# Optimization experiments

Measured on AMD Instinct MI355X. Metric: run time of the kernel, lower is better.

The kernel has to match this reference:

```python
import jax, jax.numpy as jnp
import numpy as np

B, S, D_IN = 16, 512, 768
HID, OUT = 64, 12
NEG = 1e12


def setup_inputs() -> dict:
    key = jax.random.key(0)
    k1, k2, k3 = jax.random.split(key, 3)
    x = jax.random.normal(k1, (B, S, D_IN), dtype=jnp.float32)
    mask = jnp.ones((B, S), dtype=jnp.float32)
    W = jax.random.normal(k2, (D_IN, HID * OUT * 2), dtype=jnp.float32) * 0.02
    b = jax.random.normal(k3, (HID * OUT * 2,), dtype=jnp.float32) * 0.02
    return {"x": x, "mask": mask, "W": W, "b": b}


def reference(x, mask, W, b):
    Bb, Ss, _ = x.shape
    h, out = HID, OUT
    # QKV-style projection, split into `out` heads of 2h each
    proj = (x @ W + b).reshape(Bb, Ss, out, 2 * h)  # [b, s, out, 2h]
    qw, kw = proj[..., :h], proj[..., h:]           # [b, s, out, h]

    # Sinusoidal position embedding (merge='zero'): interleaved sin/cos
    pos_ids = jnp.arange(Ss, dtype=x.dtype)
    inv_freq = jnp.power(10000.0, -2.0 * jnp.arange(h // 2, dtype=x.dtype) / h)
    ang = pos_ids[:, None] * inv_freq               # [s, h/2]
    sin, cos = jnp.sin(ang), jnp.cos(ang)
    # torch: pos[..., None, 1::2].repeat(1,1,1,2) -> TILED (not interleaved)
    cos_pos = jnp.concatenate([cos, cos], axis=-1)[None, :, None, :]  # [1, s, 1, h]
    sin_pos = jnp.concatenate([sin, sin], axis=-1)[None, :, None, :]

    def rope(w):
        # stack([-w_odd, w_even], -1).reshape -> interleaved rotation partner
        w2 = jnp.stack([-w[..., 1::2], w[..., ::2]], axis=-1).reshape(w.shape)
        return w * cos_pos + w2 * sin_pos

    qw = rope(qw)
    kw = rope(kw)

    logits = jnp.einsum('bmhd,bnhd->bhmn', qw, kw)  # [b, out, s, s]

    pad = mask[:, None, None, :]                    # broadcast over [b, out, s, s]
    logits = logits * pad - (1.0 - pad) * NEG

    tril = jnp.tril(jnp.ones((Ss, Ss), dtype=logits.dtype), -1)
    logits = logits - tril * NEG

    return logits / (h ** 0.5)
```

## Files before the change

### kernel.cpp

```cpp
#include <hip/hip_runtime.h>
#include <stdint.h>

#define DIN   768
#define NPROJ 1536
#define SEQ   512
#define NHEAD 12
#define NBATCH 16
#define NEGV  1000000000000.0f

typedef short bf16x8 __attribute__((ext_vector_type(8)));
typedef float f32x4  __attribute__((ext_vector_type(4)));

__device__ __forceinline__ unsigned short f2bf(float f) {
    union { float f; unsigned int u; } v; v.f = f;
    return (unsigned short)((v.u + 0x7FFFu + ((v.u >> 16) & 1u)) >> 16);
}
__device__ __forceinline__ float bf2f(unsigned short u) {
    union { unsigned int u; float f; } v; v.u = ((unsigned int)u) << 16;
    return v.f;
}

__global__ __launch_bounds__(256) void k_xcast(const float* __restrict__ X,
                                               unsigned short* __restrict__ Xb) {
    int i = (blockIdx.x * 256 + threadIdx.x) * 4;
    float4 v = *(const float4*)&X[i];
    short4 s;
    s.x = (short)f2bf(v.x); s.y = (short)f2bf(v.y);
    s.z = (short)f2bf(v.z); s.w = (short)f2bf(v.w);
    *(short4*)&Xb[i] = s;
}

__global__ __launch_bounds__(256) void k_wt(const float* __restrict__ W,
                                            unsigned short* __restrict__ Wt) {
    __shared__ unsigned short T[64][72];
    const int n0 = blockIdx.x * 64, k0 = blockIdx.y * 64;
    const int tid = threadIdx.x;
#pragma unroll
    for (int it = 0; it < 4; it++) {
        int c = tid + it * 256;
        int kl = c >> 4, nl = (c & 15) * 4;
        float4 v = *(const float4*)&W[(size_t)(k0 + kl) * NPROJ + n0 + nl];
        T[nl + 0][kl] = f2bf(v.x);
        T[nl + 1][kl] = f2bf(v.y);
        T[nl + 2][kl] = f2bf(v.z);
        T[nl + 3][kl] = f2bf(v.w);
    }
    __syncthreads();
#pragma unroll
    for (int it = 0; it < 2; it++) {
        int c = tid + it * 256;
        int nl = c >> 3, kb = (c & 7) * 8;
        *(int4*)&Wt[(size_t)(n0 + nl) * DIN + k0 + kb] = *(int4*)&T[nl][kb];
    }
}

template <bool PRE>
__global__ __launch_bounds__(256) void k_gemm(const float* __restrict__ X,
                                              const unsigned short* __restrict__ Xb,
                                              const unsigned short* __restrict__ Wt,
                                              const float* __restrict__ bias,
                                              unsigned short* __restrict__ P) {
    __shared__ unsigned short smem[2 * 128 * 72];
    unsigned short* sA = smem;
    unsigned short* sB = smem + 128 * 72;
    const int tid = threadIdx.x;
    const int m0 = blockIdx.y * 128, n0 = blockIdx.x * 128;
    const int lane = tid & 63, w = tid >> 6;
    const int q = lane >> 4, r = lane & 15;
    const int wm = w >> 1, wn = w & 1;
    f32x4 acc[4][4];
#pragma unroll
    for (int i = 0; i < 4; i++)
#pragma unroll
        for (int j = 0; j < 4; j++) acc[i][j] = (f32x4){0.f, 0.f, 0.f, 0.f};

    for (int k0 = 0; k0 < DIN; k0 += 64) {
        __syncthreads();
        if (PRE) {
#pragma unroll
            for (int it = 0; it < 4; it++) {
                int c = tid + it * 256;
                int row = c >> 3, col = (c & 7) * 8;
                *(int4*)&sA[row * 72 + col] =
                    *(const int4*)&Xb[(size_t)(m0 + row) * DIN + k0 + col];
            }
        } else {
#pragma unroll
            for (int it = 0; it < 8; it++) {
                int c = tid + it * 256;
                int row = c >> 4, col = (c & 15) * 4;
                float4 v = *(const float4*)&X[(size_t)(m0 + row) * DIN + k0 + col];
                short4 sv;
                sv.x = (short)f2bf(v.x); sv.y = (short)f2bf(v.y);
                sv.z = (short)f2bf(v.z); sv.w = (short)f2bf(v.w);
                *(short4*)&sA[row * 72 + col] = sv;
            }
        }
#pragma unroll
        for (int it = 0; it < 4; it++) {
            int c = tid + it * 256;
            int row = c >> 3, col = (c & 7) * 8;
            *(int4*)&sB[row * 72 + col] =
                *(const int4*)&Wt[(size_t)(n0 + row) * DIN + k0 + col];
        }
        __syncthreads();
#pragma unroll
        for (int kk = 0; kk < 64; kk += 32) {
            bf16x8 af[4], bfr[4];
#pragma unroll
            for (int t = 0; t < 4; t++)
                af[t] = *(const bf16x8*)&sA[(wm * 64 + t * 16 + r) * 72 + kk + q * 8];
#pragma unroll
            for (int t = 0; t < 4; t++)
                bfr[t] = *(const bf16x8*)&sB[(wn * 64 + t * 16 + r) * 72 + kk + q * 8];
#pragma unroll
            for (int tm = 0; tm < 4; tm++)
#pragma unroll
                for (int tn = 0; tn < 4; tn++)
                    acc[tm][tn] = __builtin_amdgcn_mfma_f32_16x16x32_bf16(
                        af[tm], bfr[tn], acc[tm][tn], 0, 0, 0);
        }
    }
    float bb[4];
#pragma unroll
    for (int tn = 0; tn < 4; tn++) bb[tn] = bias[n0 + wn * 64 + tn * 16 + r];
    __syncthreads();
    unsigned short* sT = smem;
#pragma unroll
    for (int tm = 0; tm < 4; tm++) {
        int rowb = wm * 64 + tm * 16 + q * 4;
#pragma unroll
        for (int tn = 0; tn < 4; tn++) {
            int col = wn * 64 + tn * 16 + r;
#pragma unroll
            for (int i = 0; i < 4; i++)
                sT[(rowb + i) * 136 + col] = f2bf(acc[tm][tn][i] + bb[tn]);
        }
    }
    __syncthreads();
#pragma unroll
    for (int it = 0; it < 8; it++) {
        int c = tid + it * 256;
        int row = c >> 4, colb = (c & 15) * 8;
        *(int4*)&P[(size_t)(m0 + row) * NPROJ + n0 + colb] =
            *(int4*)&sT[row * 136 + colb];
    }
}

__global__ __launch_bounds__(256) void k_rope(unsigned short* __restrict__ P) {
    const int s = blockIdx.x;
    const int tid = threadIdx.x;
    __shared__ float cs[32], sn[32];
    if (tid < 32) {
        const float C = 0.41524101186092034f;
        float a = (float)s * exp2f(-(float)tid * C);
        sincosf(a, &sn[tid], &cs[tid]);
    }
    __syncthreads();
#pragma unroll
    for (int it = 0; it < 12; it++) {
        int idx = tid + it * 256;
        int bb = idx / 192, c = idx % 192;
        unsigned short* p = P + (size_t)(bb * SEQ + s) * NPROJ + c * 8;
        union { int4 v; unsigned short u[8]; } pk;
        pk.v = *(const int4*)p;
        int d0 = (c & 7) * 8;
        float wv[8];
#pragma unroll
        for (int j = 0; j < 8; j++) wv[j] = bf2f(pk.u[j]);
#pragma unroll
        for (int pr = 0; pr < 4; pr++) {
            int je = (d0 + 2 * pr) & 31;
            int jo = je + 1;
            float oe = wv[2 * pr] * cs[je] - wv[2 * pr + 1] * sn[je];
            float oo = wv[2 * pr + 1] * cs[jo] + wv[2 * pr] * sn[jo];
            pk.u[2 * pr]     = f2bf(oe);
            pk.u[2 * pr + 1] = f2bf(oo);
        }
        *(int4*)p = pk.v;
    }
}

__global__ __launch_bounds__(256) void k_attn(const unsigned short* __restrict__ P,
                                              const float* __restrict__ mask,
                                              float* __restrict__ out) {
    __shared__ unsigned short smem[2 * 128 * 72];
    unsigned short* sQ = smem;
    unsigned short* sK = smem + 128 * 72;
    const int tid = threadIdx.x;
    const int b = blockIdx.z, h = blockIdx.y;
    const int mt = blockIdx.x >> 2, nt = blockIdx.x & 3;
#pragma unroll
    for (int it = 0; it < 4; it++) {
        int c = tid + it * 256;
        int row = c >> 3, col = (c & 7) * 8;
        size_t gq = (size_t)(b * SEQ + mt * 128 + row) * NPROJ + h * 128 + col;
        *(int4*)&sQ[row * 72 + col] = *(const int4*)&P[gq];
        size_t gk = (size_t)(b * SEQ + nt * 128 + row) * NPROJ + h * 128 + 64 + col;
        *(int4*)&sK[row * 72 + col] = *(const int4*)&P[gk];
    }
    __syncthreads();
    const int lane = tid & 63, w = tid >> 6;
    const int q = lane >> 4, r = lane & 15;
    const int wm = w >> 1, wn = w & 1;
    f32x4 acc[4][4];
#pragma unroll
    for (int i = 0; i < 4; i++)
#pragma unroll
        for (int j = 0; j < 4; j++) acc[i][j] = (f32x4){0.f, 0.f, 0.f, 0.f};
#pragma unroll
    for (int kk = 0; kk < 64; kk += 32) {
        bf16x8 af[4], bfr[4];
#pragma unroll
        for (int t = 0; t < 4; t++)
            af[t] = *(const bf16x8*)&sQ[(wm * 64 + t * 16 + r) * 72 + kk + q * 8];
#pragma unroll
        for (int t = 0; t < 4; t++)
            bfr[t] = *(const bf16x8*)&sK[(wn * 64 + t * 16 + r) * 72 + kk + q * 8];
#pragma unroll
        for (int tm = 0; tm < 4; tm++)
#pragma unroll
            for (int tn = 0; tn < 4; tn++)
                acc[tm][tn] = __builtin_amdgcn_mfma_f32_16x16x32_bf16(
                    af[tm], bfr[tn], acc[tm][tn], 0, 0, 0);
    }
    float* sbuf = (float*)smem;
    const int rowb = wm * 16 + q * 4;
#pragma unroll
    for (int tm = 0; tm < 4; tm++) {
        __syncthreads();
#pragma unroll
        for (int tn = 0; tn < 4; tn++) {
            int col = wn * 64 + tn * 16 + r;
#pragma unroll
            for (int i = 0; i < 4; i++)
                sbuf[(rowb + i) * 132 + col] = acc[tm][tn][i];
        }
        __syncthreads();
#pragma unroll
        for (int it = 0; it < 4; it++) {
            int c = tid + it * 256;
            int rl = c >> 5, cb = (c & 31) * 4;
            float4 v = *(float4*)&sbuf[rl * 132 + cb];
            int m = mt * 128 + (rl >> 4) * 64 + tm * 16 + (rl & 15);
            int n = nt * 128 + cb;
            float4 mk = *(const float4*)&mask[b * SEQ + n];
            float4 o;
            o.x = (v.x * mk.x - (1.f - mk.x) * NEGV - ((n + 0) < m ? NEGV : 0.f)) * 0.125f;
            o.y = (v.y * mk.y - (1.f - mk.y) * NEGV - ((n + 1) < m ? NEGV : 0.f)) * 0.125f;
            o.z = (v.z * mk.z - (1.f - mk.z) * NEGV - ((n + 2) < m ? NEGV : 0.f)) * 0.125f;
            o.w = (v.w * mk.w - (1.f - mk.w) * NEGV - ((n + 3) < m ? NEGV : 0.f)) * 0.125f;
            *(float4*)&out[((size_t)((b * NHEAD + h) * SEQ + m)) * SEQ + n] = o;
        }
    }
}

extern "C" void kernel_launch(void* const* d_in, const int* in_sizes, int n_in,
                              void* d_out, int out_size, void* d_ws, size_t ws_size,
                              hipStream_t stream) {
    const float* x    = (const float*)d_in[0];
    const float* mask = (const float*)d_in[1];
    const float* W    = (const float*)d_in[2];
    const float* bias = (const float*)d_in[3];
    float* out = (float*)d_out;

    const size_t wtN = (size_t)NPROJ * DIN;
    const size_t pN  = (size_t)NBATCH * SEQ * NPROJ;
    const size_t xN  = (size_t)NBATCH * SEQ * DIN;
    unsigned short* Wt = (unsigned short*)d_ws;
    unsigned short* P  = Wt + wtN;
    unsigned short* Xb = P + pN;
    const bool pre = ws_size >= (wtN + pN + xN) * sizeof(unsigned short);

    k_wt<<<dim3(NPROJ / 64, DIN / 64), 256, 0, stream>>>(W, Wt);
    if (pre) {
        k_xcast<<<(int)(xN / (256 * 4)), 256, 0, stream>>>(x, Xb);
        k_gemm<true><<<dim3(NPROJ / 128, (NBATCH * SEQ) / 128), 256, 0, stream>>>(
            x, Xb, Wt, bias, P);
    } else {
        k_gemm<false><<<dim3(NPROJ / 128, (NBATCH * SEQ) / 128), 256, 0, stream>>>(
            x, nullptr, Wt, bias, P);
    }
    k_rope<<<SEQ, 256, 0, stream>>>(P);
    k_attn<<<dim3(16, NHEAD, NBATCH), 256, 0, stream>>>(P, mask, out);
}
```

Measured before the change: 280.1 us.

## Fuse RoPE into GEMM epilogue, skip matmul for masked tiles, nontemporal stores

Removes the separate RoPE pass over P by precomputing a cos/sin table in a tiny kernel and applying the rotation in the projection GEMM's store epilogue. In the logits kernel, tiles lying entirely below the diagonal (nt<mt) skip the Q/K loads and MFMA work and write only the mask-derived constant. Output stores become nontemporal to reduce cache pollution on the large fp32 output. The skip relies on the tril term dominating, so the dot product is dropped where its contribution would vanish next to -1e12.

Measured after the change: 277.0 us. Within noise of the previous version (-1.1%).

```diff
diff --git a/kernel.cpp b/kernel.cpp
--- a/kernel.cpp
+++ b/kernel.cpp
@@ -18,6 +18,16 @@
 __device__ __forceinline__ float bf2f(unsigned short u) {
     union { unsigned int u; float f; } v; v.u = ((unsigned int)u) << 16;
     return v.f;
+}
+
+__global__ __launch_bounds__(256) void k_trig(float* __restrict__ trig) {
+    int gi = blockIdx.x * 256 + threadIdx.x;
+    int ss = gi >> 5, j = gi & 31;
+    const float C = 0.41524101186092034f;
+    float cs, sn;
+    sincosf((float)ss * exp2f(-(float)j * C), &sn, &cs);
+    trig[2 * gi]     = cs;
+    trig[2 * gi + 1] = sn;
 }
 
 __global__ __launch_bounds__(256) void k_xcast(const float* __restrict__ X,
@@ -59,6 +69,7 @@
                                               const unsigned short* __restrict__ Xb,
                                               const unsigned short* __restrict__ Wt,
                                               const float* __restrict__ bias,
+                                              const float* __restrict__ trig,
                                               unsigned short* __restrict__ P) {
     __shared__ unsigned short smem[2 * 128 * 72];
     unsigned short* sA = smem;
@@ -142,42 +153,24 @@
     for (int it = 0; it < 8; it++) {
         int c = tid + it * 256;
         int row = c >> 4, colb = (c & 15) * 8;
-        *(int4*)&P[(size_t)(m0 + row) * NPROJ + n0 + colb] =
-            *(int4*)&sT[row * 136 + colb];
-    }
-}
-
-__global__ __launch_bounds__(256) void k_rope(unsigned short* __restrict__ P) {
-    const int s = blockIdx.x;
-    const int tid = threadIdx.x;
-    __shared__ float cs[32], sn[32];
-    if (tid < 32) {
-        const float C = 0.41524101186092034f;
-        float a = (float)s * exp2f(-(float)tid * C);
-        sincosf(a, &sn[tid], &cs[tid]);
-    }
-    __syncthreads();
-#pragma unroll
-    for (int it = 0; it < 12; it++) {
-        int idx = tid + it * 256;
-        int bb = idx / 192, c = idx % 192;
-        unsigned short* p = P + (size_t)(bb * SEQ + s) * NPROJ + c * 8;
+        int m = m0 + row;
+        int s = m & (SEQ - 1);
+        int base = colb & 31;
         union { int4 v; unsigned short u[8]; } pk;
-        pk.v = *(const int4*)p;
-        int d0 = (c & 7) * 8;
+        pk.v = *(int4*)&sT[row * 136 + colb];
         float wv[8];
 #pragma unroll
         for (int j = 0; j < 8; j++) wv[j] = bf2f(pk.u[j]);
-#pragma unroll
-        for (int pr = 0; pr < 4; pr++) {
-            int je = (d0 + 2 * pr) & 31;
-            int jo = je + 1;
-            float oe = wv[2 * pr] * cs[je] - wv[2 * pr + 1] * sn[je];
-            float oo = wv[2 * pr + 1] * cs[jo] + wv[2 * pr] * sn[jo];
-            pk.u[2 * pr]     = f2bf(oe);
-            pk.u[2 * pr + 1] = f2bf(oo);
-        }
-        *(int4*)p = pk.v;
+        const float* tp = &trig[2 * (s * 32 + base)];
+#pragma unroll
+        for (int p = 0; p < 4; p++) {
+            float4 tt = *(const float4*)&tp[4 * p];
+            float oe = wv[2 * p] * tt.x - wv[2 * p + 1] * tt.y;
+            float oo = wv[2 * p + 1] * tt.z + wv[2 * p] * tt.w;
+            pk.u[2 * p]     = f2bf(oe);
+            pk.u[2 * p + 1] = f2bf(oo);
+        }
+        *(int4*)&P[(size_t)m * NPROJ + n0 + colb] = pk.v;
     }
 }
 
@@ -190,6 +183,24 @@
     const int tid = threadIdx.x;
     const int b = blockIdx.z, h = blockIdx.y;
     const int mt = blockIdx.x >> 2, nt = blockIdx.x & 3;
+    const size_t obase = ((size_t)((b * NHEAD + h) * SEQ)) * SEQ;
+
+    if (nt < mt) {
+#pragma unroll
+        for (int it = 0; it < 16; it++) {
+            int c = tid + it * 256;
+            int rl = c >> 5, cb = (c & 31) * 4;
+            int m = mt * 128 + rl, n = nt * 128 + cb;
+            f32x4 mk = *(const f32x4*)&mask[b * SEQ + n];
+            f32x4 o;
+#pragma unroll
+            for (int j = 0; j < 4; j++)
+                o[j] = (-(1.f - mk[j]) * NEGV - NEGV) * 0.125f;
+            __builtin_nontemporal_store(o, (f32x4*)&out[obase + (size_t)m * SEQ + n]);
+        }
+        return;
+    }
+
 #pragma unroll
     for (int it = 0; it < 4; it++) {
         int c = tid + it * 256;
@@ -241,16 +252,16 @@
         for (int it = 0; it < 4; it++) {
             int c = tid + it * 256;
             int rl = c >> 5, cb = (c & 31) * 4;
-            float4 v = *(float4*)&sbuf[rl * 132 + cb];
+            f32x4 v = *(f32x4*)&sbuf[rl * 132 + cb];
             int m = mt * 128 + (rl >> 4) * 64 + tm * 16 + (rl & 15);
             int n = nt * 128 + cb;
-            float4 mk = *(const float4*)&mask[b * SEQ + n];
-            float4 o;
-            o.x = (v.x * mk.x - (1.f - mk.x) * NEGV - ((n + 0) < m ? NEGV : 0.f)) * 0.125f;
-            o.y = (v.y * mk.y - (1.f - mk.y) * NEGV - ((n + 1) < m ? NEGV : 0.f)) * 0.125f;
-            o.z = (v.z * mk.z - (1.f - mk.z) * NEGV - ((n + 2) < m ? NEGV : 0.f)) * 0.125f;
-            o.w = (v.w * mk.w - (1.f - mk.w) * NEGV - ((n + 3) < m ? NEGV : 0.f)) * 0.125f;
-            *(float4*)&out[((size_t)((b * NHEAD + h) * SEQ + m)) * SEQ + n] = o;
+            f32x4 mk = *(const f32x4*)&mask[b * SEQ + n];
+            f32x4 o;
+#pragma unroll
+            for (int j = 0; j < 4; j++)
+                o[j] = (v[j] * mk[j] - (1.f - mk[j]) * NEGV
+                        - ((n + j) < m ? NEGV : 0.f)) * 0.125f;
+            __builtin_nontemporal_store(o, (f32x4*)&out[obase + (size_t)m * SEQ + n]);
         }
     }
 }
@@ -267,20 +278,24 @@
     const size_t wtN = (size_t)NPROJ * DIN;
     const size_t pN  = (size_t)NBATCH * SEQ * NPROJ;
     const size_t xN  = (size_t)NBATCH * SEQ * DIN;
+    const size_t trigN = (size_t)SEQ * 32 * 2;
     unsigned short* Wt = (unsigned short*)d_ws;
     unsigned short* P  = Wt + wtN;
-    unsigned short* Xb = P + pN;
-    const bool pre = ws_size >= (wtN + pN + xN) * sizeof(unsigned short);
-
+    float* trig        = (float*)(P + pN);
+    unsigned short* Xb = (unsigned short*)(trig + trigN);
+    const bool pre = ws_size >= (wtN + pN) * sizeof(unsigned short)
+                               + trigN * sizeof(float)
+                               + xN * sizeof(unsigned short);
+
+    k_trig<<<SEQ * 32 / 256, 256, 0, stream>>>(trig);
     k_wt<<<dim3(NPROJ / 64, DIN / 64), 256, 0, stream>>>(W, Wt);
     if (pre) {
         k_xcast<<<(int)(xN / (256 * 4)), 256, 0, stream>>>(x, Xb);
         k_gemm<true><<<dim3(NPROJ / 128, (NBATCH * SEQ) / 128), 256, 0, stream>>>(
-            x, Xb, Wt, bias, P);
+            x, Xb, Wt, bias, trig, P);
     } else {
         k_gemm<false><<<dim3(NPROJ / 128, (NBATCH * SEQ) / 128), 256, 0, stream>>>(
-            x, nullptr, Wt, bias, P);
-    }
-    k_rope<<<SEQ, 256, 0, stream>>>(P);
+            x, nullptr, Wt, bias, trig, P);
+    }
     k_attn<<<dim3(16, NHEAD, NBATCH), 256, 0, stream>>>(P, mask, out);
 }
```
